# Performance work log

Hardware: AMD Instinct MI355X
Metric: run time of the kernel (lower is better)

Reference implementation:

```python
import jax, jax.numpy as jnp
import numpy as np

H = 1024          # rnn hidden dim
D = H // 2        # coarse/fine half
E = H // 8        # embed dim = 128
COND = H // 2     # conditioning (upsampled mel) dim = 512
EPS = 1e-5
TILE = 16


def _bn(x, scale, offset):
    # haiku BatchNorm, training mode: batch stats over (N, L)
    mean = jnp.mean(x, axis=(0, 1), keepdims=True)
    var = jnp.mean(jnp.square(x), axis=(0, 1), keepdims=True) - jnp.square(mean)
    return scale * (x - mean) * jax.lax.rsqrt(var + EPS) + offset


def _conv(x, w, rate=1):
    return jax.lax.conv_general_dilated(
        x, w, window_strides=(1,), padding='VALID', rhs_dilation=(rate,),
        dimension_numbers=('NWC', 'WIO', 'NWC'))


def _up(x, w, stride):
    # Conv1DTranspose with kernel 1, SAME padding: scatter x@w to positions i*stride
    N, L, _ = x.shape
    y = jnp.einsum('nlc,cd->nld', x, w)
    out = jnp.zeros((N, L, stride, y.shape[-1]), y.dtype).at[:, :, 0, :].set(y)
    return out.reshape(N, L * stride, y.shape[-1])


def _iw_mask():
    m = jnp.ones((COND + 3 * E, 3 * H), jnp.float32)
    for j in (0, 2, 4):  # coarse_t embed cannot see coarse half of u, r, e gates
        m = m.at[-E:, j * D:(j + 1) * D].set(0.0)
    return m


def _forward(x, mel, conv_in_w, bn0_s, bn0_o, dconv1_w, bn1_s, bn1_o,
             dconv2_w, bn2_s, bn2_o, up1_w, bn3_s, bn3_o, up2_w, bn4_s, bn4_o,
             up3_w, bn5_s, bn5_o, I_W, I_b, R_w, R_b,
             O1_w, O1_b, O2_w, O2_b, O3_w, O3_b, O4_w, O4_b, c_embed, f_embed):
    # ---- UpsampleNetwork ----
    h = jax.nn.relu(_bn(_conv(mel, conv_in_w), bn0_s, bn0_o))
    r1 = jax.nn.relu(_bn(_conv(h, dconv1_w, rate=2), bn1_s, bn1_o))
    h = h[:, 1:-1] + r1
    r2 = jax.nn.relu(_bn(_conv(h, dconv2_w, rate=4), bn2_s, bn2_o))
    h = h[:, 2:-2] + r2
    h = jax.nn.relu(_bn(_up(h, up1_w, 2), bn3_s, bn3_o))
    h = jax.nn.relu(_bn(_up(h, up2_w, 2), bn4_s, bn4_o))
    h = jax.nn.relu(_bn(_up(h, up3_w, 4), bn5_s, bn5_o))
    N, Lm, Dm = h.shape
    mel_up = jnp.tile(h[:, :, None, :], (1, 1, TILE, 1)).reshape(N, Lm * TILE, Dm)

    # ---- WaveRNNOriginal.__call__ (teacher-forced GRU) ----
    coarse, fine, coarse_t = x[..., 0], x[..., 1], x[..., 2]
    inputs = jnp.concatenate(
        (mel_up, c_embed[coarse], f_embed[fine], c_embed[coarse_t]), axis=-1)
    # precompute input projection for all timesteps  [N, L, 3H]
    ix = jnp.einsum('nli,ij->nlj', inputs, I_W * _iw_mask()) + I_b.reshape(1, 1, -1)
    ix_t = jnp.swapaxes(ix, 0, 1)  # time-major [L, N, 3H]
    h0 = jnp.zeros((N, H), ix.dtype)

    def step(hx, xt):
        u1, r1_, e1 = jnp.split(hx @ R_w + R_b, 3, axis=-1)
        u2, r2_, e2 = jnp.split(xt, 3, axis=-1)
        ut = jax.nn.sigmoid(u1 + u2)
        rt = jax.nn.sigmoid(r1_ + r2_)
        et = jnp.tanh(rt * e1 + e2)
        ht = ut * hx + (1.0 - ut) * et
        return ht, ht

    _, hs = jax.lax.scan(step, h0, ix_t)
    hs = jnp.swapaxes(hs, 0, 1)              # [N, L, H]
    yc, yf = jnp.split(hs, 2, axis=-1)       # [N, L, H/2] each
    clog = jax.nn.relu(yc @ O1_w + O1_b) @ O2_w + O2_b
    flog = jax.nn.relu(yf @ O3_w + O3_b) @ O4_w + O4_b
    logits = jnp.stack((clog, flog), axis=-1)  # [N, L, 256, 2]
    return jax.nn.log_softmax(logits, axis=-2)


def setup_inputs():
    key = jax.random.key(0)
    ks = jax.random.split(key, 24)
    n = jax.random.normal
    N, T = 2, 24
    L = (T - 8) * 256  # 4096
    inp = {
        'x': jax.random.randint(ks[0], (N, L, 3), 0, 256),
        'mel': n(ks[1], (N, T, 80), jnp.float32),
        'conv_in_w': n(ks[2], (3, 80, 512)) * 0.05,
        'dconv1_w': n(ks[3], (2, 512, 512)) * 0.05,
        'dconv2_w': n(ks[4], (2, 512, 512)) * 0.05,
        'up1_w': n(ks[5], (512, 512)) * 0.05,
        'up2_w': n(ks[6], (512, 512)) * 0.05,
        'up3_w': n(ks[7], (512, COND)) * 0.05,
        'I_W': n(ks[8], (COND + 3 * E, 3 * H)) * 0.03,
        'I_b': jnp.zeros((3 * H,)),
        'R_w': n(ks[9], (H, 3 * H)) * 0.03,
        'R_b': jnp.zeros((3 * H,)),
        'O1_w': n(ks[10], (D, D)) * 0.05,
        'O1_b': jnp.zeros((D,)),
        'O2_w': n(ks[11], (D, 256)) * 0.05,
        'O2_b': jnp.zeros((256,)),
        'O3_w': n(ks[12], (D, D)) * 0.05,
        'O3_b': jnp.zeros((D,)),
        'O4_w': n(ks[13], (D, 256)) * 0.05,
        'O4_b': jnp.zeros((256,)),
        'c_embed': n(ks[14], (256, E)) * 0.1,
        'f_embed': n(ks[15], (256, E)) * 0.1,
    }
    for i in range(6):
        c = COND if i == 5 else 512
        inp[f'bn{i}_s'] = jnp.ones((c,))
        inp[f'bn{i}_o'] = jnp.zeros((c,))
    return inp


def reference(x, mel, conv_in_w, dconv1_w, dconv2_w, up1_w, up2_w, up3_w,
              I_W, I_b, R_w, R_b, O1_w, O1_b, O2_w, O2_b, O3_w, O3_b,
              O4_w, O4_b, c_embed, f_embed,
              bn0_s, bn0_o, bn1_s, bn1_o, bn2_s, bn2_o,
              bn3_s, bn3_o, bn4_s, bn4_o, bn5_s, bn5_o):
    return _forward(x, mel, conv_in_w, bn0_s, bn0_o, dconv1_w, bn1_s, bn1_o,
                    dconv2_w, bn2_s, bn2_o, up1_w, bn3_s, bn3_o, up2_w, bn4_s,
                    bn4_o, up3_w, bn5_s, bn5_o, I_W, I_b, R_w, R_b,
                    O1_w, O1_b, O2_w, O2_b, O3_w, O3_b, O4_w, O4_b,
                    c_embed, f_embed)
```

## Files before the change

kernel.cpp:

```cpp
#include <hip/hip_runtime.h>
#include <hip/hip_bf16.h>
#include <math.h>

__device__ __forceinline__ float bf2f(unsigned short u) {
  unsigned int x = ((unsigned int)u) << 16;
  return __builtin_bit_cast(float, x);
}
__device__ __forceinline__ unsigned short f2bf(float f) {
  unsigned int x = __builtin_bit_cast(unsigned int, f);
  unsigned int lsb = (x >> 16) & 1u;
  x += 0x7fffu + lsb;
  return (unsigned short)(x >> 16);
}
template <bool BF>
__device__ __forceinline__ float ld(const void* p, size_t i) {
  if (BF) return bf2f(((const unsigned short*)p)[i]);
  return ((const float*)p)[i];
}

#define SCOPE_AGENT __HIP_MEMORY_SCOPE_AGENT
typedef unsigned long long ull;

__global__ void k_init(const unsigned int* bn0s, ull* sbuf, int* dt) {
  int t = threadIdx.x;
  for (int i = t; i < 4096; i += 256) sbuf[i] = 0ULL;
  if (t == 0) dt[0] = (bn0s[0] == 0x3F803F80u) ? 1 : 0;
}

template <bool BF>
__device__ void conv_in_body(const void* mel, const void* w, float* out) {
  int idx = blockIdx.x * 256 + threadIdx.x;
  if (idx >= 2 * 22 * 512) return;
  int c = idx & 511, l = (idx >> 9) % 22, n = idx / (22 * 512);
  float acc = 0.f;
  for (int kw = 0; kw < 3; kw++) {
    size_t mrow = (size_t)(n * 24 + l + kw) * 80;
    size_t wrow = (size_t)kw * 80 * 512 + c;
#pragma unroll 4
    for (int i = 0; i < 80; i++)
      acc += ld<BF>(mel, mrow + i) * ld<BF>(w, wrow + (size_t)i * 512);
  }
  out[idx] = acc;
}
__global__ void k_conv_in(const void* mel, const void* w, float* out, const int* dt) {
  if (dt[0]) conv_in_body<true>(mel, w, out); else conv_in_body<false>(mel, w, out);
}

template <bool BF>
__device__ void dconv_body(const float* in, const void* w, float* out,
                           int Lin, int Lout, int rate) {
  int idx = blockIdx.x * 256 + threadIdx.x;
  if (idx >= 2 * Lout * 512) return;
  int c = idx & 511, l = (idx >> 9) % Lout, n = idx / (Lout * 512);
  float acc = 0.f;
  for (int kw = 0; kw < 2; kw++) {
    const float* irow = in + (n * Lin + l + kw * rate) * 512;
    size_t wrow = (size_t)kw * 512 * 512 + c;
#pragma unroll 4
    for (int i = 0; i < 512; i++)
      acc += irow[i] * ld<BF>(w, wrow + (size_t)i * 512);
  }
  out[idx] = acc;
}
__global__ void k_dconv(const float* in, const void* w, float* out,
                        int Lin, int Lout, int rate, const int* dt) {
  if (dt[0]) dconv_body<true>(in, w, out, Lin, Lout, rate);
  else dconv_body<false>(in, w, out, Lin, Lout, rate);
}

template <bool BF>
__device__ void up_body(const float* in, const void* w, float* out, int Lin, int stride) {
  int Lout = Lin * stride;
  int idx = blockIdx.x * 256 + threadIdx.x;
  if (idx >= 2 * Lout * 512) return;
  int c = idx & 511, lo = (idx >> 9) % Lout, n = idx / (Lout * 512);
  if (lo % stride) { out[idx] = 0.f; return; }
  const float* irow = in + (n * Lin + lo / stride) * 512;
  float acc = 0.f;
#pragma unroll 4
  for (int i = 0; i < 512; i++) acc += irow[i] * ld<BF>(w, (size_t)i * 512 + c);
  out[idx] = acc;
}
__global__ void k_up(const float* in, const void* w, float* out,
                     int Lin, int stride, const int* dt) {
  if (dt[0]) up_body<true>(in, w, out, Lin, stride);
  else up_body<false>(in, w, out, Lin, stride);
}

__global__ void k_bnstats(const float* __restrict__ x, float* __restrict__ st, int NL) {
  int c = blockIdx.x * 256 + threadIdx.x;
  if (c >= 512) return;
  float s = 0.f, s2 = 0.f;
  for (int r = 0; r < NL; r++) { float v = x[r * 512 + c]; s += v; s2 += v * v; }
  float m = s / (float)NL;
  float var = s2 / (float)NL - m * m;
  st[c] = m;
  st[512 + c] = rsqrtf(var + 1e-5f);
}

template <bool BF>
__device__ void bnrelu_body(const float* x, float* y, const float* st,
                            const void* sc, const void* of,
                            const float* res, int resL, int shift, int L) {
  int idx = blockIdx.x * 256 + threadIdx.x;
  if (idx >= 2 * L * 512) return;
  int c = idx & 511, l = (idx >> 9) % L, n = idx / (L * 512);
  float v = (x[idx] - st[c]) * st[512 + c] * ld<BF>(sc, c) + ld<BF>(of, c);
  v = fmaxf(v, 0.f);
  if (res) v += res[(n * resL + l + shift) * 512 + c];
  y[idx] = v;
}
__global__ void k_bnrelu(const float* x, float* y, const float* st,
                         const void* sc, const void* of,
                         const float* res, int resL, int shift, int L, const int* dt) {
  if (dt[0]) bnrelu_body<true>(x, y, st, sc, of, res, resL, shift, L);
  else bnrelu_body<false>(x, y, st, sc, of, res, resL, shift, L);
}

template <bool BF>
__device__ void M_body(const float* h5, const void* IW, const void* Ib,
                       const void* Rb, float* M, float* hl) {
  int bid = blockIdx.x;
  int rt = bid / 12, ct = bid % 12;
  int r0 = rt * 8, j = ct * 256 + threadIdx.x;
  const float4* src = (const float4*)(h5 + (size_t)r0 * 512);
  float4* dst = (float4*)hl;
  for (int q = threadIdx.x; q < 1024; q += 256) dst[q] = src[q];
  __syncthreads();
  float acc[8];
#pragma unroll
  for (int r = 0; r < 8; r++) acc[r] = 0.f;
  for (int k = 0; k < 512; k += 4) {
    float w0 = ld<BF>(IW, (size_t)k * 3072 + j);
    float w1 = ld<BF>(IW, (size_t)(k + 1) * 3072 + j);
    float w2 = ld<BF>(IW, (size_t)(k + 2) * 3072 + j);
    float w3 = ld<BF>(IW, (size_t)(k + 3) * 3072 + j);
#pragma unroll
    for (int r = 0; r < 8; r++) {
      float4 h4 = *(const float4*)(hl + r * 512 + k);
      acc[r] += h4.x * w0 + h4.y * w1 + h4.z * w2 + h4.w * w3;
    }
  }
  float bias = ld<BF>(Ib, j) + ((j < 2048) ? ld<BF>(Rb, j) : 0.f);
#pragma unroll
  for (int r = 0; r < 8; r++) M[(size_t)(r0 + r) * 3072 + j] = acc[r] + bias;
}
__global__ __launch_bounds__(256) void k_M(const float* h5, const void* IW,
                                           const void* Ib, const void* Rb,
                                           float* M, const int* dt) {
  __shared__ float hl[8 * 512];
  if (dt[0]) M_body<true>(h5, IW, Ib, Rb, M, hl);
  else M_body<false>(h5, IW, Ib, Rb, M, hl);
}

template <bool BF>
__device__ void T_body(const void* emb, const void* IW, int row0, int maskcoarse,
                       float* T, float* el) {
  int bid = blockIdx.x;
  int vt = bid / 12, ct = bid % 12;
  int v0 = vt * 8, j = ct * 256 + threadIdx.x;
  for (int q = threadIdx.x; q < 1024; q += 256)
    el[q] = ld<BF>(emb, (size_t)v0 * 128 + q);
  __syncthreads();
  float acc[8];
#pragma unroll
  for (int r = 0; r < 8; r++) acc[r] = 0.f;
  for (int k = 0; k < 128; k += 4) {
    float w0 = ld<BF>(IW, (size_t)(row0 + k) * 3072 + j);
    float w1 = ld<BF>(IW, (size_t)(row0 + k + 1) * 3072 + j);
    float w2 = ld<BF>(IW, (size_t)(row0 + k + 2) * 3072 + j);
    float w3 = ld<BF>(IW, (size_t)(row0 + k + 3) * 3072 + j);
#pragma unroll
    for (int r = 0; r < 8; r++) {
      float4 e4 = *(const float4*)(el + r * 128 + k);
      acc[r] += e4.x * w0 + e4.y * w1 + e4.z * w2 + e4.w * w3;
    }
  }
  bool mask = maskcoarse && ((j & 1023) < 512);
#pragma unroll
  for (int r = 0; r < 8; r++)
    T[(size_t)(v0 + r) * 3072 + j] = mask ? 0.f : acc[r];
}
__global__ __launch_bounds__(256) void k_T(const void* emb, const void* IW, int row0,
                                           int maskcoarse, float* T, const int* dt) {
  __shared__ float el[8 * 128];
  if (dt[0]) T_body<true>(emb, IW, row0, maskcoarse, T, el);
  else T_body<false>(emb, IW, row0, maskcoarse, T, el);
}

#define NWG 128
template <bool BF>
__device__ void gru_body(const float* __restrict__ M, const float* __restrict__ T1,
                         const float* __restrict__ T2, const float* __restrict__ T3,
                         const int* __restrict__ x, const void* Rw, const void* Rb,
                         ull* sbuf, unsigned short* __restrict__ hs, float* hlds) {
  const int g = blockIdx.x, tid = threadIdx.x;
  const int n = g >> 6;
  const int il = tid >> 5, ks = tid & 31;
  const int i = (g & 63) * 16 + il;
  const int koff = ks * 32;
  const int k0 = tid * 2;
  const int lidx = (k0 >> 6) * 68 + (k0 & 63);

  float wreg[96];
#pragma unroll
  for (int gt = 0; gt < 3; gt++)
#pragma unroll
    for (int kk = 0; kk < 32; kk++)
      wreg[gt * 32 + kk] = ld<BF>(Rw, (size_t)(koff + kk) * 3072 + gt * 1024 + i);
  const float rbe = ld<BF>(Rb, 2048 + i);

  float hprev = 0.f;

  for (int t = 0; t < 4096; t++) {
    float au = 0.f, ar = 0.f, ae = 0.f;
    if (ks == 0) {
      const int* xr = x + (n * 4096 + t) * 3;
      int ci = xr[0], fi = xr[1], cti = xr[2];
      const float* mr = M + (size_t)(n * 256 + (t >> 4)) * 3072;
      const float* p1 = T1 + (size_t)ci * 3072;
      const float* p2 = T2 + (size_t)fi * 3072;
      const float* p3 = T3 + (size_t)cti * 3072;
      au = mr[i] + p1[i] + p2[i] + p3[i];
      ar = mr[1024 + i] + p1[1024 + i] + p2[1024 + i] + p3[1024 + i];
      ae = mr[2048 + i] + p1[2048 + i] + p2[2048 + i] + p3[2048 + i];
    }

    const ull thr = (ull)(unsigned int)t << 32;
    ull* sb = sbuf + (size_t)(((t & 1) << 1) + n) * 1024 + k0;
    ull s0, s1;
    while (true) {
      s0 = __hip_atomic_load(sb + 0, __ATOMIC_RELAXED, SCOPE_AGENT);
      s1 = __hip_atomic_load(sb + 1, __ATOMIC_RELAXED, SCOPE_AGENT);
      if (s0 >= thr && s1 >= thr) break;
    }
    float2 h2;
    h2.x = __builtin_bit_cast(float, (unsigned int)s0);
    h2.y = __builtin_bit_cast(float, (unsigned int)s1);
    *(float2*)(hlds + lidx) = h2;
    __syncthreads();

    float du = 0.f, dr = 0.f, de = 0.f;
    const float* hp = hlds + (ks >> 1) * 68 + (ks & 1) * 32;
#pragma unroll
    for (int kk = 0; kk < 32; kk += 4) {
      float4 h4 = *(const float4*)(hp + kk);
      du += wreg[kk] * h4.x + wreg[kk + 1] * h4.y + wreg[kk + 2] * h4.z + wreg[kk + 3] * h4.w;
      dr += wreg[32 + kk] * h4.x + wreg[33 + kk] * h4.y + wreg[34 + kk] * h4.z + wreg[35 + kk] * h4.w;
      de += wreg[64 + kk] * h4.x + wreg[65 + kk] * h4.y + wreg[66 + kk] * h4.z + wreg[67 + kk] * h4.w;
    }
#pragma unroll
    for (int off = 16; off > 0; off >>= 1) {
      du += __shfl_xor(du, off, 32);
      dr += __shfl_xor(dr, off, 32);
      de += __shfl_xor(de, off, 32);
    }

    if (ks == 0) {
      float u = 1.f / (1.f + __expf(-(du + au)));
      float r = 1.f / (1.f + __expf(-(dr + ar)));
      float w = r * (de + rbe) + ae;
      float e = 1.f - 2.f / (__expf(2.f * w) + 1.f);
      float ht = u * hprev + (1.f - u) * e;
      hprev = ht;
      ull slot = ((ull)(unsigned int)(t + 1) << 32) |
                 (ull)__builtin_bit_cast(unsigned int, ht);
      __hip_atomic_store(
          sbuf + (size_t)((((t + 1) & 1) << 1) + n) * 1024 + i, slot,
          __ATOMIC_RELAXED, SCOPE_AGENT);
      hs[(size_t)(n * 4096 + t) * 1024 + i] = f2bf(ht);
    }
    __syncthreads();
  }
}
__global__ __launch_bounds__(512, 1) void k_gru(
    const float* M, const float* T1, const float* T2, const float* T3,
    const int* x, const void* Rw, const void* Rb,
    ull* sbuf, unsigned short* hs, const int* dt) {
  __shared__ __align__(16) float hlds[16 * 68];
  if (dt[0]) gru_body<true>(M, T1, T2, T3, x, Rw, Rb, sbuf, hs, hlds);
  else gru_body<false>(M, T1, T2, T3, x, Rw, Rb, sbuf, hs, hlds);
}

template <bool BF>
__device__ void out1_body(const unsigned short* __restrict__ hs,
                          const void* O1w, const void* O1b,
                          const void* O3w, const void* O3b,
                          unsigned short* __restrict__ tmid, unsigned short* lds) {
  int b = blockIdx.x, tid = threadIdx.x;
  size_t r0 = (size_t)b * 16;
  const uint4* src = (const uint4*)(hs + r0 * 1024);
  uint4* dst = (uint4*)lds;
  for (int q = tid; q < 2048; q += 256) dst[q] = src[q];
  __syncthreads();

  float acc[4][16];
#pragma unroll
  for (int jg = 0; jg < 4; jg++)
#pragma unroll
    for (int r = 0; r < 16; r++) acc[jg][r] = 0.f;

  for (int k = 0; k < 512; k++) {
    float w0 = ld<BF>(O1w, (size_t)k * 512 + tid);
    float w1 = ld<BF>(O1w, (size_t)k * 512 + 256 + tid);
    float w2 = ld<BF>(O3w, (size_t)k * 512 + tid);
    float w3 = ld<BF>(O3w, (size_t)k * 512 + 256 + tid);
#pragma unroll
    for (int r = 0; r < 16; r++) {
      float hc = bf2f(lds[r * 1024 + k]);
      float hf = bf2f(lds[r * 1024 + 512 + k]);
      acc[0][r] += hc * w0; acc[1][r] += hc * w1;
      acc[2][r] += hf * w2; acc[3][r] += hf * w3;
    }
  }
  float bia[4] = { ld<BF>(O1b, tid), ld<BF>(O1b, 256 + tid),
                   ld<BF>(O3b, tid), ld<BF>(O3b, 256 + tid) };
#pragma unroll
  for (int jg = 0; jg < 4; jg++)
#pragma unroll
    for (int r = 0; r < 16; r++) {
      float v = fmaxf(acc[jg][r] + bia[jg], 0.f);
      tmid[(r0 + r) * 1024 + jg * 256 + tid] = f2bf(v);
    }
}
__global__ __launch_bounds__(256) void k_out1(
    const unsigned short* hs, const void* O1w, const void* O1b,
    const void* O3w, const void* O3b, unsigned short* tmid, const int* dt) {
  __shared__ unsigned short lds[16 * 1024];
  if (dt[0]) out1_body<true>(hs, O1w, O1b, O3w, O3b, tmid, lds);
  else out1_body<false>(hs, O1w, O1b, O3w, O3b, tmid, lds);
}

__device__ __forceinline__ float blkmax(float v, float* red, int tid) {
#pragma unroll
  for (int off = 32; off > 0; off >>= 1) v = fmaxf(v, __shfl_xor(v, off));
  __syncthreads();
  if ((tid & 63) == 0) red[tid >> 6] = v;
  __syncthreads();
  return fmaxf(fmaxf(red[0], red[1]), fmaxf(red[2], red[3]));
}
__device__ __forceinline__ float blksum(float v, float* red, int tid) {
#pragma unroll
  for (int off = 32; off > 0; off >>= 1) v += __shfl_xor(v, off);
  __syncthreads();
  if ((tid & 63) == 0) red[tid >> 6] = v;
  __syncthreads();
  return red[0] + red[1] + red[2] + red[3];
}

template <bool BF>
__device__ void out2_body(const unsigned short* __restrict__ tmid,
                          const void* O2w, const void* O2b,
                          const void* O4w, const void* O4b,
                          void* out, unsigned short* lds, float* red) {
  int b = blockIdx.x, tid = threadIdx.x, q = tid;
  size_t r0 = (size_t)b * 16;
  const uint4* src = (const uint4*)(tmid + r0 * 1024);
  uint4* dst = (uint4*)lds;
  for (int p = tid; p < 2048; p += 256) dst[p] = src[p];
  __syncthreads();

  float ac[16], af[16];
#pragma unroll
  for (int r = 0; r < 16; r++) { ac[r] = 0.f; af[r] = 0.f; }
  for (int j = 0; j < 512; j++) {
    float w2 = ld<BF>(O2w, (size_t)j * 256 + q);
    float w4 = ld<BF>(O4w, (size_t)j * 256 + q);
#pragma unroll
    for (int r = 0; r < 16; r++) {
      ac[r] += bf2f(lds[r * 1024 + j]) * w2;
      af[r] += bf2f(lds[r * 1024 + 512 + j]) * w4;
    }
  }
  float b2 = ld<BF>(O2b, q), b4 = ld<BF>(O4b, q);
  for (int r = 0; r < 16; r++) {
    float c = ac[r] + b2;
    float f = af[r] + b4;
    float mc = blkmax(c, red, tid);
    float sc = blksum(__expf(c - mc), red, tid);
    float mf = blkmax(f, red, tid);
    float sf = blksum(__expf(f - mf), red, tid);
    size_t row = r0 + r;
    float oc = c - mc - logf(sc);
    float of_ = f - mf - logf(sf);
    if (BF) {
      ((unsigned short*)out)[(row * 256 + q) * 2 + 0] = f2bf(oc);
      ((unsigned short*)out)[(row * 256 + q) * 2 + 1] = f2bf(of_);
    } else {
      ((float*)out)[(row * 256 + q) * 2 + 0] = oc;
      ((float*)out)[(row * 256 + q) * 2 + 1] = of_;
    }
  }
}
__global__ __launch_bounds__(256) void k_out2(
    const unsigned short* tmid, const void* O2w, const void* O2b,
    const void* O4w, const void* O4b, void* out, const int* dt) {
  __shared__ unsigned short lds[16 * 1024];
  __shared__ float red[8];
  if (dt[0]) out2_body<true>(tmid, O2w, O2b, O4w, O4b, out, lds, red);
  else out2_body<false>(tmid, O2w, O2b, O4w, O4b, out, lds, red);
}

extern "C" void kernel_launch(void* const* d_in, const int* in_sizes, int n_in,
                              void* d_out, int out_size, void* d_ws, size_t ws_size,
                              hipStream_t stream) {
  const int* x = (const int*)d_in[0];
  const void* mel = d_in[1];
  const void* conv_in_w = d_in[2];
  const void* dconv1_w = d_in[3];
  const void* dconv2_w = d_in[4];
  const void* up1_w = d_in[5];
  const void* up2_w = d_in[6];
  const void* up3_w = d_in[7];
  const void* IW = d_in[8];
  const void* Ib = d_in[9];
  const void* Rw = d_in[10];
  const void* Rb = d_in[11];
  const void* O1w = d_in[12];
  const void* O1b = d_in[13];
  const void* O2w = d_in[14];
  const void* O2b = d_in[15];
  const void* O3w = d_in[16];
  const void* O3b = d_in[17];
  const void* O4w = d_in[18];
  const void* O4b = d_in[19];
  const void* c_embed = d_in[20];
  const void* f_embed = d_in[21];
  const void* bns[6], *bno[6];
  for (int s = 0; s < 6; s++) {
    bns[s] = d_in[22 + 2 * s];
    bno[s] = d_in[23 + 2 * s];
  }

  float* ws = (float*)d_ws;
  float* A = ws;
  float* B = A + 262144;
  float* st = B + 262144;
  float* M = st + 1024;
  float* T1 = M + 1572864;
  float* T2 = T1 + 786432;
  float* T3 = T2 + 786432;
  ull* sbuf = (ull*)(T3 + 786432);
  int* dt = (int*)(sbuf + 4096);
  unsigned short* hs = (unsigned short*)(dt + 4);
  unsigned short* tmid = hs + 8388608;

  k_init<<<1, 256, 0, stream>>>((const unsigned int*)bns[0], sbuf, dt);

  k_conv_in<<<88, 256, 0, stream>>>(mel, conv_in_w, A, dt);
  k_bnstats<<<2, 256, 0, stream>>>(A, st, 44);
  k_bnrelu<<<88, 256, 0, stream>>>(A, A, st, bns[0], bno[0], nullptr, 0, 0, 22, dt);

  k_dconv<<<80, 256, 0, stream>>>(A, dconv1_w, B, 22, 20, 2, dt);
  k_bnstats<<<2, 256, 0, stream>>>(B, st, 40);
  k_bnrelu<<<80, 256, 0, stream>>>(B, B, st, bns[1], bno[1], A, 22, 1, 20, dt);

  k_dconv<<<64, 256, 0, stream>>>(B, dconv2_w, A, 20, 16, 4, dt);
  k_bnstats<<<2, 256, 0, stream>>>(A, st, 32);
  k_bnrelu<<<64, 256, 0, stream>>>(A, A, st, bns[2], bno[2], B, 20, 2, 16, dt);

  k_up<<<128, 256, 0, stream>>>(A, up1_w, B, 16, 2, dt);
  k_bnstats<<<2, 256, 0, stream>>>(B, st, 64);
  k_bnrelu<<<128, 256, 0, stream>>>(B, B, st, bns[3], bno[3], nullptr, 0, 0, 32, dt);

  k_up<<<256, 256, 0, stream>>>(B, up2_w, A, 32, 2, dt);
  k_bnstats<<<2, 256, 0, stream>>>(A, st, 128);
  k_bnrelu<<<256, 256, 0, stream>>>(A, A, st, bns[4], bno[4], nullptr, 0, 0, 64, dt);

  k_up<<<1024, 256, 0, stream>>>(A, up3_w, B, 64, 4, dt);
  k_bnstats<<<2, 256, 0, stream>>>(B, st, 512);
  k_bnrelu<<<1024, 256, 0, stream>>>(B, B, st, bns[5], bno[5], nullptr, 0, 0, 256, dt);

  k_M<<<768, 256, 0, stream>>>(B, IW, Ib, Rb, M, dt);
  k_T<<<384, 256, 0, stream>>>(c_embed, IW, 512, 0, T1, dt);
  k_T<<<384, 256, 0, stream>>>(f_embed, IW, 640, 0, T2, dt);
  k_T<<<384, 256, 0, stream>>>(c_embed, IW, 768, 1, T3, dt);

  k_gru<<<NWG, 512, 0, stream>>>(M, T1, T2, T3, x, Rw, Rb, sbuf, hs, dt);

  k_out1<<<512, 256, 0, stream>>>(hs, O1w, O1b, O3w, O3b, tmid, dt);
  k_out2<<<512, 256, 0, stream>>>(tmid, O2w, O2b, O4w, O4b, d_out, dt);

  (void)in_sizes; (void)n_in; (void)out_size; (void)ws_size;
}
```

Measured before the change: 9.246 ms.

## Poll hidden state with one wave and publish via single wave

Instead of all 512 threads spinning on the global sequence-tagged hidden buffer, only wave 0 polls (16 contiguous slots per lane), first spinning on one slot and then reading all 16. The updated hidden values from the 16 row-owner lanes are gathered in shared memory and stored to global by a single wave. This aims to cut global polling traffic and contention on the per-step cross-workgroup barrier. The cost is an extra __syncthreads per step and serialized polling through one wave.

```diff
diff --git a/kernel.cpp b/kernel.cpp
--- a/kernel.cpp
+++ b/kernel.cpp
@@ -193,14 +193,15 @@
 __device__ void gru_body(const float* __restrict__ M, const float* __restrict__ T1,
                          const float* __restrict__ T2, const float* __restrict__ T3,
                          const int* __restrict__ x, const void* Rw, const void* Rb,
-                         ull* sbuf, unsigned short* __restrict__ hs, float* hlds) {
+                         ull* sbuf, unsigned short* __restrict__ hs,
+                         float* hlds, float* hpub) {
   const int g = blockIdx.x, tid = threadIdx.x;
   const int n = g >> 6;
+  const int wgid = g & 63;
+  const int wave = tid >> 6, lane = tid & 63;
   const int il = tid >> 5, ks = tid & 31;
-  const int i = (g & 63) * 16 + il;
+  const int i = wgid * 16 + il;
   const int koff = ks * 32;
-  const int k0 = tid * 2;
-  const int lidx = (k0 >> 6) * 68 + (k0 & 63);
 
   float wreg[96];
 #pragma unroll
@@ -209,6 +210,8 @@
     for (int kk = 0; kk < 32; kk++)
       wreg[gt * 32 + kk] = ld<BF>(Rw, (size_t)(koff + kk) * 3072 + gt * 1024 + i);
   const float rbe = ld<BF>(Rb, 2048 + i);
+
+  const int lb = ((lane * 16) >> 6) * 68 + ((lane * 16) & 63);
 
   float hprev = 0.f;
 
@@ -226,18 +229,32 @@
       ae = mr[2048 + i] + p1[2048 + i] + p2[2048 + i] + p3[2048 + i];
     }
 
-    const ull thr = (ull)(unsigned int)t << 32;
-    ull* sb = sbuf + (size_t)(((t & 1) << 1) + n) * 1024 + k0;
-    ull s0, s1;
-    while (true) {
-      s0 = __hip_atomic_load(sb + 0, __ATOMIC_RELAXED, SCOPE_AGENT);
-      s1 = __hip_atomic_load(sb + 1, __ATOMIC_RELAXED, SCOPE_AGENT);
-      if (s0 >= thr && s1 >= thr) break;
-    }
-    float2 h2;
-    h2.x = __builtin_bit_cast(float, (unsigned int)s0);
-    h2.y = __builtin_bit_cast(float, (unsigned int)s1);
-    *(float2*)(hlds + lidx) = h2;
+    if (wave == 0) {
+      ull* sb = sbuf + (size_t)(((t & 1) << 1) + n) * 1024 + lane * 16;
+      const ull thr = (ull)(unsigned int)t << 32;
+      while (__hip_atomic_load(sb, __ATOMIC_RELAXED, SCOPE_AGENT) < thr) {}
+      float hv[16];
+      while (true) {
+        ull s[16];
+#pragma unroll
+        for (int j = 0; j < 16; j++)
+          s[j] = __hip_atomic_load(sb + j, __ATOMIC_RELAXED, SCOPE_AGENT);
+        bool ok = true;
+#pragma unroll
+        for (int j = 0; j < 16; j++) ok &= (s[j] >= thr);
+        if (ok) {
+#pragma unroll
+          for (int j = 0; j < 16; j++)
+            hv[j] = __builtin_bit_cast(float, (unsigned int)s[j]);
+          break;
+        }
+      }
+#pragma unroll
+      for (int q = 0; q < 4; q++) {
+        float4 v = make_float4(hv[4 * q], hv[4 * q + 1], hv[4 * q + 2], hv[4 * q + 3]);
+        *(float4*)(hlds + lb + 4 * q) = v;
+      }
+    }
     __syncthreads();
 
     float du = 0.f, dr = 0.f, de = 0.f;
@@ -263,14 +280,19 @@
       float e = 1.f - 2.f / (__expf(2.f * w) + 1.f);
       float ht = u * hprev + (1.f - u) * e;
       hprev = ht;
+      hpub[il] = ht;
+    }
+    __syncthreads();
+
+    if (wave == 0 && lane < 16) {
+      float ht = hpub[lane];
       ull slot = ((ull)(unsigned int)(t + 1) << 32) |
                  (ull)__builtin_bit_cast(unsigned int, ht);
       __hip_atomic_store(
-          sbuf + (size_t)((((t + 1) & 1) << 1) + n) * 1024 + i, slot,
+          sbuf + (size_t)((((t + 1) & 1) << 1) + n) * 1024 + wgid * 16 + lane, slot,
           __ATOMIC_RELAXED, SCOPE_AGENT);
-      hs[(size_t)(n * 4096 + t) * 1024 + i] = f2bf(ht);
-    }
-    __syncthreads();
+      hs[(size_t)(n * 4096 + t) * 1024 + wgid * 16 + lane] = f2bf(ht);
+    }
   }
 }
 __global__ __launch_bounds__(512, 1) void k_gru(
@@ -278,8 +300,9 @@
     const int* x, const void* Rw, const void* Rb,
     ull* sbuf, unsigned short* hs, const int* dt) {
   __shared__ __align__(16) float hlds[16 * 68];
-  if (dt[0]) gru_body<true>(M, T1, T2, T3, x, Rw, Rb, sbuf, hs, hlds);
-  else gru_body<false>(M, T1, T2, T3, x, Rw, Rb, sbuf, hs, hlds);
+  __shared__ float hpub[16];
+  if (dt[0]) gru_body<true>(M, T1, T2, T3, x, Rw, Rb, sbuf, hs, hlds, hpub);
+  else gru_body<false>(M, T1, T2, T3, x, Rw, Rb, sbuf, hs, hlds, hpub);
 }
 
 template <bool BF>
```

Result: slower. 11.84 ms (+28.1%).

## Fuse output MLP and log-softmax into GRU kernel as concurrent consumer workgroups

Applied to the files above, without the earlier changes.

Adds 128 extra workgroups to the persistent GRU launch. They spin on flag-tagged hidden-state words (bf16 value packed with timestep+1) and compute the O1/O3, O2/O4 and log-softmax epilogue per row while the recurrence is still running, replacing the two separate output kernels. The GRU loop now double-buffers its shared-memory staging and drops its trailing barrier, and the hidden-state buffer is zeroed by a new kernel. The aim is to hide the epilogue behind the latency-bound recurrence. The risks are that epilogue blocks compete for CUs and memory bandwidth with the GRU, that the epilogue runs per row with poor weight reuse, and that co-residency of all 256 blocks is needed to avoid deadlock.

```diff
diff --git a/kernel.cpp b/kernel.cpp
--- a/kernel.cpp
+++ b/kernel.cpp
@@ -25,6 +25,9 @@
   int t = threadIdx.x;
   for (int i = t; i < 4096; i += 256) sbuf[i] = 0ULL;
   if (t == 0) dt[0] = (bn0s[0] == 0x3F803F80u) ? 1 : 0;
+}
+__global__ void k_zero(uint4* hq4) {
+  hq4[(size_t)blockIdx.x * 256 + threadIdx.x] = make_uint4(0u, 0u, 0u, 0u);
 }
 
 template <bool BF>
@@ -189,11 +192,12 @@
 }
 
 #define NWG 128
+#define NEPI 128
 template <bool BF>
 __device__ void gru_body(const float* __restrict__ M, const float* __restrict__ T1,
                          const float* __restrict__ T2, const float* __restrict__ T3,
                          const int* __restrict__ x, const void* Rw, const void* Rb,
-                         ull* sbuf, unsigned short* __restrict__ hs, float* hlds) {
+                         ull* sbuf, unsigned int* __restrict__ hq, float* hlds) {
   const int g = blockIdx.x, tid = threadIdx.x;
   const int n = g >> 6;
   const int il = tid >> 5, ks = tid & 31;
@@ -213,6 +217,8 @@
   float hprev = 0.f;
 
   for (int t = 0; t < 4096; t++) {
+    float* hb = hlds + (t & 1) * (16 * 68);
+
     float au = 0.f, ar = 0.f, ae = 0.f;
     if (ks == 0) {
       const int* xr = x + (n * 4096 + t) * 3;
@@ -237,11 +243,11 @@
     float2 h2;
     h2.x = __builtin_bit_cast(float, (unsigned int)s0);
     h2.y = __builtin_bit_cast(float, (unsigned int)s1);
-    *(float2*)(hlds + lidx) = h2;
+    *(float2*)(hb + lidx) = h2;
     __syncthreads();
 
     float du = 0.f, dr = 0.f, de = 0.f;
-    const float* hp = hlds + (ks >> 1) * 68 + (ks & 1) * 32;
+    const float* hp = hb + (ks >> 1) * 68 + (ks & 1) * 32;
 #pragma unroll
     for (int kk = 0; kk < 32; kk += 4) {
       float4 h4 = *(const float4*)(hp + kk);
@@ -268,137 +274,102 @@
       __hip_atomic_store(
           sbuf + (size_t)((((t + 1) & 1) << 1) + n) * 1024 + i, slot,
           __ATOMIC_RELAXED, SCOPE_AGENT);
-      hs[(size_t)(n * 4096 + t) * 1024 + i] = f2bf(ht);
-    }
-    __syncthreads();
-  }
-}
+      unsigned int hv = ((unsigned int)f2bf(ht) << 16) | (unsigned int)(t + 1);
+      __hip_atomic_store(hq + (size_t)(n * 4096 + t) * 1024 + i, hv,
+                         __ATOMIC_RELAXED, SCOPE_AGENT);
+    }
+  }
+}
+
+template <bool BF>
+__device__ void epi_body(const unsigned int* __restrict__ hq,
+                         const void* O1w, const void* O1b,
+                         const void* O3w, const void* O3b,
+                         const void* O2w, const void* O2b,
+                         const void* O4w, const void* O4b,
+                         void* out, float* smem) {
+  const int e = blockIdx.x - NWG, tid = threadIdx.x;
+  float* hrow = smem;
+  float* tmid = smem + 1024;
+  float* red = smem + 2048;
+  const int col = tid & 255;
+  const bool isf = tid >= 256;
+  const int base = isf ? 4 : 0;
+  const void* W2 = isf ? O4w : O2w;
+  const float b2 = isf ? ld<BF>(O4b, col) : ld<BF>(O2b, col);
+
+  for (int tc = 0; tc < 32; tc++) {
+    int t = tc * NEPI + e;
+    for (int n = 0; n < 2; n++) {
+      size_t row = (size_t)n * 4096 + t;
+      const unsigned int* hp = hq + row * 1024 + tid * 2;
+      unsigned int a, b;
+      while (true) {
+        a = __hip_atomic_load(hp + 0, __ATOMIC_RELAXED, SCOPE_AGENT);
+        b = __hip_atomic_load(hp + 1, __ATOMIC_RELAXED, SCOPE_AGENT);
+        if ((a & 0xffffu) && (b & 0xffffu)) break;
+        __builtin_amdgcn_s_sleep(16);
+      }
+      float2 h2;
+      h2.x = __builtin_bit_cast(float, a & 0xffff0000u);
+      h2.y = __builtin_bit_cast(float, b & 0xffff0000u);
+      *(float2*)(hrow + tid * 2) = h2;
+      __syncthreads();
+
+      float a1 = 0.f, a3 = 0.f;
+#pragma unroll 4
+      for (int k = 0; k < 512; k++) {
+        a1 += hrow[k] * ld<BF>(O1w, (size_t)k * 512 + tid);
+        a3 += hrow[512 + k] * ld<BF>(O3w, (size_t)k * 512 + tid);
+      }
+      tmid[tid] = fmaxf(a1 + ld<BF>(O1b, tid), 0.f);
+      tmid[512 + tid] = fmaxf(a3 + ld<BF>(O3b, tid), 0.f);
+      __syncthreads();
+
+      float acc = 0.f;
+      const float* tm = tmid + (isf ? 512 : 0);
+#pragma unroll 4
+      for (int j = 0; j < 512; j++)
+        acc += tm[j] * ld<BF>(W2, (size_t)j * 256 + col);
+      acc += b2;
+
+      float v = acc;
+#pragma unroll
+      for (int off = 32; off > 0; off >>= 1) v = fmaxf(v, __shfl_xor(v, off));
+      if ((tid & 63) == 0) red[tid >> 6] = v;
+      __syncthreads();
+      float m = fmaxf(fmaxf(red[base], red[base + 1]),
+                      fmaxf(red[base + 2], red[base + 3]));
+      __syncthreads();
+      float s = __expf(acc - m);
+#pragma unroll
+      for (int off = 32; off > 0; off >>= 1) s += __shfl_xor(s, off);
+      if ((tid & 63) == 0) red[tid >> 6] = s;
+      __syncthreads();
+      float ssum = red[base] + red[base + 1] + red[base + 2] + red[base + 3];
+      float o = acc - m - logf(ssum);
+      __syncthreads();
+      if (BF) ((unsigned short*)out)[(row * 256 + col) * 2 + (isf ? 1 : 0)] = f2bf(o);
+      else ((float*)out)[(row * 256 + col) * 2 + (isf ? 1 : 0)] = o;
+    }
+  }
+}
+
 __global__ __launch_bounds__(512, 1) void k_gru(
     const float* M, const float* T1, const float* T2, const float* T3,
     const int* x, const void* Rw, const void* Rb,
-    ull* sbuf, unsigned short* hs, const int* dt) {
-  __shared__ __align__(16) float hlds[16 * 68];
-  if (dt[0]) gru_body<true>(M, T1, T2, T3, x, Rw, Rb, sbuf, hs, hlds);
-  else gru_body<false>(M, T1, T2, T3, x, Rw, Rb, sbuf, hs, hlds);
-}
-
-template <bool BF>
-__device__ void out1_body(const unsigned short* __restrict__ hs,
-                          const void* O1w, const void* O1b,
-                          const void* O3w, const void* O3b,
-                          unsigned short* __restrict__ tmid, unsigned short* lds) {
-  int b = blockIdx.x, tid = threadIdx.x;
-  size_t r0 = (size_t)b * 16;
-  const uint4* src = (const uint4*)(hs + r0 * 1024);
-  uint4* dst = (uint4*)lds;
-  for (int q = tid; q < 2048; q += 256) dst[q] = src[q];
-  __syncthreads();
-
-  float acc[4][16];
-#pragma unroll
-  for (int jg = 0; jg < 4; jg++)
-#pragma unroll
-    for (int r = 0; r < 16; r++) acc[jg][r] = 0.f;
-
-  for (int k = 0; k < 512; k++) {
-    float w0 = ld<BF>(O1w, (size_t)k * 512 + tid);
-    float w1 = ld<BF>(O1w, (size_t)k * 512 + 256 + tid);
-    float w2 = ld<BF>(O3w, (size_t)k * 512 + tid);
-    float w3 = ld<BF>(O3w, (size_t)k * 512 + 256 + tid);
-#pragma unroll
-    for (int r = 0; r < 16; r++) {
-      float hc = bf2f(lds[r * 1024 + k]);
-      float hf = bf2f(lds[r * 1024 + 512 + k]);
-      acc[0][r] += hc * w0; acc[1][r] += hc * w1;
-      acc[2][r] += hf * w2; acc[3][r] += hf * w3;
-    }
-  }
-  float bia[4] = { ld<BF>(O1b, tid), ld<BF>(O1b, 256 + tid),
-                   ld<BF>(O3b, tid), ld<BF>(O3b, 256 + tid) };
-#pragma unroll
-  for (int jg = 0; jg < 4; jg++)
-#pragma unroll
-    for (int r = 0; r < 16; r++) {
-      float v = fmaxf(acc[jg][r] + bia[jg], 0.f);
-      tmid[(r0 + r) * 1024 + jg * 256 + tid] = f2bf(v);
-    }
-}
-__global__ __launch_bounds__(256) void k_out1(
-    const unsigned short* hs, const void* O1w, const void* O1b,
-    const void* O3w, const void* O3b, unsigned short* tmid, const int* dt) {
-  __shared__ unsigned short lds[16 * 1024];
-  if (dt[0]) out1_body<true>(hs, O1w, O1b, O3w, O3b, tmid, lds);
-  else out1_body<false>(hs, O1w, O1b, O3w, O3b, tmid, lds);
-}
-
-__device__ __forceinline__ float blkmax(float v, float* red, int tid) {
-#pragma unroll
-  for (int off = 32; off > 0; off >>= 1) v = fmaxf(v, __shfl_xor(v, off));
-  __syncthreads();
-  if ((tid & 63) == 0) red[tid >> 6] = v;
-  __syncthreads();
-  return fmaxf(fmaxf(red[0], red[1]), fmaxf(red[2], red[3]));
-}
-__device__ __forceinline__ float blksum(float v, float* red, int tid) {
-#pragma unroll
-  for (int off = 32; off > 0; off >>= 1) v += __shfl_xor(v, off);
-  __syncthreads();
-  if ((tid & 63) == 0) red[tid >> 6] = v;
-  __syncthreads();
-  return red[0] + red[1] + red[2] + red[3];
-}
-
-template <bool BF>
-__device__ void out2_body(const unsigned short* __restrict__ tmid,
-                          const void* O2w, const void* O2b,
-                          const void* O4w, const void* O4b,
-                          void* out, unsigned short* lds, float* red) {
-  int b = blockIdx.x, tid = threadIdx.x, q = tid;
-  size_t r0 = (size_t)b * 16;
-  const uint4* src = (const uint4*)(tmid + r0 * 1024);
-  uint4* dst = (uint4*)lds;
-  for (int p = tid; p < 2048; p += 256) dst[p] = src[p];
-  __syncthreads();
-
-  float ac[16], af[16];
-#pragma unroll
-  for (int r = 0; r < 16; r++) { ac[r] = 0.f; af[r] = 0.f; }
-  for (int j = 0; j < 512; j++) {
-    float w2 = ld<BF>(O2w, (size_t)j * 256 + q);
-    float w4 = ld<BF>(O4w, (size_t)j * 256 + q);
-#pragma unroll
-    for (int r = 0; r < 16; r++) {
-      ac[r] += bf2f(lds[r * 1024 + j]) * w2;
-      af[r] += bf2f(lds[r * 1024 + 512 + j]) * w4;
-    }
-  }
-  float b2 = ld<BF>(O2b, q), b4 = ld<BF>(O4b, q);
-  for (int r = 0; r < 16; r++) {
-    float c = ac[r] + b2;
-    float f = af[r] + b4;
-    float mc = blkmax(c, red, tid);
-    float sc = blksum(__expf(c - mc), red, tid);
-    float mf = blkmax(f, red, tid);
-    float sf = blksum(__expf(f - mf), red, tid);
-    size_t row = r0 + r;
-    float oc = c - mc - logf(sc);
-    float of_ = f - mf - logf(sf);
-    if (BF) {
-      ((unsigned short*)out)[(row * 256 + q) * 2 + 0] = f2bf(oc);
-      ((unsigned short*)out)[(row * 256 + q) * 2 + 1] = f2bf(of_);
-    } else {
-      ((float*)out)[(row * 256 + q) * 2 + 0] = oc;
-      ((float*)out)[(row * 256 + q) * 2 + 1] = of_;
-    }
-  }
-}
-__global__ __launch_bounds__(256) void k_out2(
-    const unsigned short* tmid, const void* O2w, const void* O2b,
-    const void* O4w, const void* O4b, void* out, const int* dt) {
-  __shared__ unsigned short lds[16 * 1024];
-  __shared__ float red[8];
-  if (dt[0]) out2_body<true>(tmid, O2w, O2b, O4w, O4b, out, lds, red);
-  else out2_body<false>(tmid, O2w, O2b, O4w, O4b, out, lds, red);
+    ull* sbuf, unsigned int* hq,
+    const void* O1w, const void* O1b, const void* O3w, const void* O3b,
+    const void* O2w, const void* O2b, const void* O4w, const void* O4b,
+    void* out, const int* dt) {
+  __shared__ __align__(16) float smem[2176];
+  if (dt[0]) {
+    if (blockIdx.x < NWG) gru_body<true>(M, T1, T2, T3, x, Rw, Rb, sbuf, hq, smem);
+    else epi_body<true>(hq, O1w, O1b, O3w, O3b, O2w, O2b, O4w, O4b, out, smem);
+  } else {
+    if (blockIdx.x < NWG) gru_body<false>(M, T1, T2, T3, x, Rw, Rb, sbuf, hq, smem);
+    else epi_body<false>(hq, O1w, O1b, O3w, O3b, O2w, O2b, O4w, O4b, out, smem);
+  }
 }
 
 extern "C" void kernel_launch(void* const* d_in, const int* in_sizes, int n_in,
@@ -442,10 +413,10 @@
   float* T3 = T2 + 786432;
   ull* sbuf = (ull*)(T3 + 786432);
   int* dt = (int*)(sbuf + 4096);
-  unsigned short* hs = (unsigned short*)(dt + 4);
-  unsigned short* tmid = hs + 8388608;
+  unsigned int* hq = (unsigned int*)(dt + 4);
 
   k_init<<<1, 256, 0, stream>>>((const unsigned int*)bns[0], sbuf, dt);
+  k_zero<<<8192, 256, 0, stream>>>((uint4*)hq);
 
   k_conv_in<<<88, 256, 0, stream>>>(mel, conv_in_w, A, dt);
   k_bnstats<<<2, 256, 0, stream>>>(A, st, 44);
@@ -476,10 +447,9 @@
   k_T<<<384, 256, 0, stream>>>(f_embed, IW, 640, 0, T2, dt);
   k_T<<<384, 256, 0, stream>>>(c_embed, IW, 768, 1, T3, dt);
 
-  k_gru<<<NWG, 512, 0, stream>>>(M, T1, T2, T3, x, Rw, Rb, sbuf, hs, dt);
-
-  k_out1<<<512, 256, 0, stream>>>(hs, O1w, O1b, O3w, O3b, tmid, dt);
-  k_out2<<<512, 256, 0, stream>>>(tmid, O2w, O2b, O4w, O4b, d_out, dt);
+  k_gru<<<NWG + NEPI, 512, 0, stream>>>(M, T1, T2, T3, x, Rw, Rb, sbuf, hq,
+                                        O1w, O1b, O3w, O3b, O2w, O2b, O4w, O4b,
+                                        d_out, dt);
 
   (void)in_sizes; (void)n_in; (void)out_size; (void)ws_size;
 }
```

New measurement: 9.622 ms. 4.1% more time.
